# Kernel tuning notes

Measured on AMD Instinct MI355X. Metric: run time of the kernel, lower is better.

Reference implementation:

```python
import jax, jax.numpy as jnp
import numpy as np

N_NODES = 100000
N_EDGES = 640000
H_FEATS = 128


def setup_inputs() -> dict:
    key = jax.random.key(0)
    k_h, k_src, k_dst, k_w1, k_b1, k_w2, k_b2 = jax.random.split(key, 7)
    h = jax.random.normal(k_h, (N_NODES, H_FEATS), dtype=jnp.float32)
    src = jax.random.randint(k_src, (N_EDGES,), 0, N_NODES, dtype=jnp.int64)
    dst = jax.random.randint(k_dst, (N_EDGES,), 0, N_NODES, dtype=jnp.int64)
    # nn.Linear params: W1 (h_feats, 2*h_feats) as (out, in); store transposed for x @ W
    lim1 = 1.0 / np.sqrt(2 * H_FEATS)
    W1 = jax.random.uniform(k_w1, (2 * H_FEATS, H_FEATS), jnp.float32, -lim1, lim1)
    b1 = jax.random.uniform(k_b1, (H_FEATS,), jnp.float32, -lim1, lim1)
    lim2 = 1.0 / np.sqrt(H_FEATS)
    W2 = jax.random.uniform(k_w2, (H_FEATS, 1), jnp.float32, -lim2, lim2)
    b2 = jax.random.uniform(k_b2, (1,), jnp.float32, -lim2, lim2)
    return {"h": h, "src": src, "dst": dst, "W1": W1, "b1": b1, "W2": W2, "b2": b2}


def reference(h, src, dst, W1, b1, W2, b2):
    # gather src/dst node features per edge and concat: [E, 2*h_feats]
    he = jnp.concatenate([h[src], h[dst]], axis=1)
    hidden = jax.nn.relu(he @ W1 + b1)          # [E, h_feats]
    score = (hidden @ W2 + b2)[:, 0]            # [E]
    return score
```

## Files before the change

### kernel.cpp

```cpp
#include <hip/hip_runtime.h>

#define N_NODES 100000
#define N_EDGES 640000
#define F 128
#define NT 6250

typedef __attribute__((ext_vector_type(8))) short short8;
typedef __attribute__((ext_vector_type(4))) float float4v;

static __device__ __forceinline__ unsigned short f2bf(float f) {
    unsigned int u = __float_as_uint(f);
    u += 0x7fffu + ((u >> 16) & 1u);
    return (unsigned short)(u >> 16);
}

__global__ __launch_bounds__(256) void prep_wt(
    const float* __restrict__ W1, unsigned short* __restrict__ Wt)
{
    int id = blockIdx.x * 256 + threadIdx.x;
    int n = id >> 7, k = id & 127;
    float v = W1[((n & 128) + k) * 128 + (n & 127)];
    Wt[id] = f2bf(v);
}

__global__ __launch_bounds__(256, 4) void node_proj(
    const float* __restrict__ h, const unsigned short* __restrict__ Wt,
    const float* __restrict__ b1,
    unsigned short* __restrict__ A, unsigned short* __restrict__ B)
{
    __shared__ unsigned short w_lds[128 * 136];
    __shared__ unsigned short h_lds[4][2][16 * 136];

    const int tid  = threadIdx.x;
    const int lane = tid & 63;
    const int l16  = lane & 15;
    const int quad = lane >> 4;
    const int w    = tid >> 6;
    const int y    = blockIdx.y;

#pragma unroll
    for (int i = 0; i < 8; ++i) {
        int c = i * 256 + tid;
        int r = c >> 4, cc = c & 15;
        uint4 v = *(const uint4*)(Wt + (size_t)(y * 128 + r) * F + cc * 8);
        *(uint4*)&w_lds[r * 136 + cc * 8] = v;
    }
    __syncthreads();

    unsigned short* hb0 = &h_lds[w][0][0];
    unsigned short* hb1 = &h_lds[w][1][0];
    unsigned short* outp = (y == 0) ? A : B;

    int srow[8], sc4[8];
#pragma unroll
    for (int i = 0; i < 8; ++i) { int f = i * 64 + lane; srow[i] = f >> 5; sc4[i] = f & 31; }

#define LOADH(PF, T)                                                           \
    _Pragma("unroll") for (int i = 0; i < 8; ++i)                              \
        PF[i] = *(const float4*)(h + ((size_t)(T) * 16 + srow[i]) * F + sc4[i] * 4);

#define CVTWRITE(PF, DST)                                                      \
    _Pragma("unroll") for (int i = 0; i < 8; ++i) {                            \
        uint2 p;                                                               \
        p.x = (unsigned)f2bf(PF[i].x) | ((unsigned)f2bf(PF[i].y) << 16);       \
        p.y = (unsigned)f2bf(PF[i].z) | ((unsigned)f2bf(PF[i].w) << 16);       \
        *(uint2*)&(DST)[srow[i] * 136 + sc4[i] * 4] = p;                       \
    }

    int t = blockIdx.x * 4 + w;
    bool act = (t < NT);
    float4 pf[8];
    if (act) { LOADH(pf, t); CVTWRITE(pf, hb0); }

    int buf = 0;
    while (act) {
        const int tn = t + 1024;
        const bool actn = (tn < NT);
        if (actn) LOADH(pf, tn);

        unsigned short* hb = buf ? hb1 : hb0;
        float4v acc[8];
#pragma unroll
        for (int mt = 0; mt < 8; ++mt) acc[mt] = (float4v){0.f, 0.f, 0.f, 0.f};
#pragma unroll
        for (int k0 = 0; k0 < 4; ++k0) {
            const int kb = k0 * 32 + quad * 8;
            short8 bf = *(const short8*)&hb[l16 * 136 + kb];
#pragma unroll
            for (int mt = 0; mt < 8; ++mt) {
                short8 af = *(const short8*)&w_lds[(mt * 16 + l16) * 136 + kb];
                acc[mt] = __builtin_amdgcn_mfma_f32_16x16x32_bf16(af, bf, acc[mt], 0, 0, 0);
            }
        }

        if (actn) CVTWRITE(pf, buf ? hb0 : hb1);

        {
            const size_t nodeoff = ((size_t)t * 16 + l16) * F;
#pragma unroll
            for (int mt = 0; mt < 8; ++mt) {
                const int col = mt * 16 + quad * 4;
                float4 bv = make_float4(0.f, 0.f, 0.f, 0.f);
                if (y == 0) bv = *(const float4*)(b1 + col);
                ushort4 sv;
                sv.x = f2bf(acc[mt][0] + bv.x);
                sv.y = f2bf(acc[mt][1] + bv.y);
                sv.z = f2bf(acc[mt][2] + bv.z);
                sv.w = f2bf(acc[mt][3] + bv.w);
                *(ushort4*)(outp + nodeoff + col) = sv;
            }
        }
        buf ^= 1; t = tn; act = actn;
    }
#undef LOADH
#undef CVTWRITE
}

__global__ __launch_bounds__(256) void edge_score(
    const unsigned short* __restrict__ A, const unsigned short* __restrict__ B,
    const int* __restrict__ src, const int* __restrict__ dst,
    const float* __restrict__ W2, const float* __restrict__ b2,
    float* __restrict__ out)
{
    const int tid = threadIdx.x;
    const int sub = tid & 7;
    const int e0  = blockIdx.x * 128 + (tid >> 3) * 4;
    const int j0  = sub * 16;

    const int4 sv = *(const int4*)(src + e0);
    const int4 dv = *(const int4*)(dst + e0);
    const int s[4] = {sv.x, sv.y, sv.z, sv.w};
    const int d[4] = {dv.x, dv.y, dv.z, dv.w};

    uint4 av0[4], av1[4], bv0[4], bv1[4];
#pragma unroll
    for (int i = 0; i < 4; ++i) {
        const uint4* Ap = (const uint4*)(A + (size_t)s[i] * F + j0);
        const uint4* Bp = (const uint4*)(B + (size_t)d[i] * F + j0);
        av0[i] = Ap[0]; av1[i] = Ap[1];
        bv0[i] = Bp[0]; bv1[i] = Bp[1];
    }

    const float4* Wp = (const float4*)(W2 + j0);
    const float4 w0 = Wp[0], w1 = Wp[1], w2 = Wp[2], w3 = Wp[3];
    const float bias = b2[0];

#define TERM(UA, UB, WL, WH)                                                   \
    {                                                                          \
        float fa0 = __uint_as_float((UA) << 16);                               \
        float fa1 = __uint_as_float((UA) & 0xFFFF0000u);                       \
        float fb0 = __uint_as_float((UB) << 16);                               \
        float fb1 = __uint_as_float((UB) & 0xFFFF0000u);                       \
        sacc = fmaf(fmaxf(fa0 + fb0, 0.f), (WL), sacc);                        \
        sacc = fmaf(fmaxf(fa1 + fb1, 0.f), (WH), sacc);                        \
    }
#pragma unroll
    for (int i = 0; i < 4; ++i) {
        float sacc = 0.f;
        TERM(av0[i].x, bv0[i].x, w0.x, w0.y)
        TERM(av0[i].y, bv0[i].y, w0.z, w0.w)
        TERM(av0[i].z, bv0[i].z, w1.x, w1.y)
        TERM(av0[i].w, bv0[i].w, w1.z, w1.w)
        TERM(av1[i].x, bv1[i].x, w2.x, w2.y)
        TERM(av1[i].y, bv1[i].y, w2.z, w2.w)
        TERM(av1[i].z, bv1[i].z, w3.x, w3.y)
        TERM(av1[i].w, bv1[i].w, w3.z, w3.w)
        sacc += __shfl_xor(sacc, 1);
        sacc += __shfl_xor(sacc, 2);
        sacc += __shfl_xor(sacc, 4);
        if (sub == 0) out[e0 + i] = sacc + bias;
    }
#undef TERM
}

extern "C" void kernel_launch(void* const* d_in, const int* in_sizes, int n_in,
                              void* d_out, int out_size, void* d_ws, size_t ws_size,
                              hipStream_t stream) {
    const float* h   = (const float*)d_in[0];
    const int*   src = (const int*)d_in[1];
    const int*   dst = (const int*)d_in[2];
    const float* W1  = (const float*)d_in[3];
    const float* b1  = (const float*)d_in[4];
    const float* W2  = (const float*)d_in[5];
    const float* b2  = (const float*)d_in[6];
    float* out = (float*)d_out;

    unsigned short* Wt = (unsigned short*)d_ws;
    unsigned short* A  = Wt + 256 * 128;
    unsigned short* B  = A + (size_t)N_NODES * F;

    prep_wt<<<128, 256, 0, stream>>>(W1, Wt);
    node_proj<<<dim3(256, 2), 256, 0, stream>>>(h, Wt, b1, A, B);
    edge_score<<<N_EDGES / 128, 256, 0, stream>>>(A, B, src, dst, W2, b2, out);
}
```

Before: 166.1 us.

## Compute both node projections in one block to read h once

node_proj now loads the full 256x128 bf16 weight into LDS and computes both the src-half (A) and dst-half (B) projections for each 16-node tile in a single pass. Previously a second grid dimension computed them separately, so every tile of h was read and converted twice. Blocks grow to 512 threads with one block per CU, and the per-wave h buffer goes from double to single buffering. This trades away some occupancy and double-buffer overlap in exchange for halving the h traffic and conversion work.

```diff
diff --git a/kernel.cpp b/kernel.cpp
--- a/kernel.cpp
+++ b/kernel.cpp
@@ -23,33 +23,35 @@
     Wt[id] = f2bf(v);
 }
 
-__global__ __launch_bounds__(256, 4) void node_proj(
+__global__ __launch_bounds__(512, 1) void node_proj(
     const float* __restrict__ h, const unsigned short* __restrict__ Wt,
     const float* __restrict__ b1,
     unsigned short* __restrict__ A, unsigned short* __restrict__ B)
 {
-    __shared__ unsigned short w_lds[128 * 136];
-    __shared__ unsigned short h_lds[4][2][16 * 136];
+    __shared__ unsigned short w_lds[256 * 136];
+    __shared__ unsigned short h_lds[8][16 * 136 + 8];
 
     const int tid  = threadIdx.x;
     const int lane = tid & 63;
     const int l16  = lane & 15;
     const int quad = lane >> 4;
     const int w    = tid >> 6;
-    const int y    = blockIdx.y;
 
 #pragma unroll
     for (int i = 0; i < 8; ++i) {
-        int c = i * 256 + tid;
+        int c = i * 512 + tid;
         int r = c >> 4, cc = c & 15;
-        uint4 v = *(const uint4*)(Wt + (size_t)(y * 128 + r) * F + cc * 8);
+        uint4 v = *(const uint4*)(Wt + (size_t)r * F + cc * 8);
         *(uint4*)&w_lds[r * 136 + cc * 8] = v;
     }
     __syncthreads();
 
-    unsigned short* hb0 = &h_lds[w][0][0];
-    unsigned short* hb1 = &h_lds[w][1][0];
-    unsigned short* outp = (y == 0) ? A : B;
+    float4 bv[8];
+#pragma unroll
+    for (int mt = 0; mt < 8; ++mt)
+        bv[mt] = *(const float4*)(b1 + mt * 16 + quad * 4);
+
+    unsigned short* hb = &h_lds[w][0];
 
     int srow[8], sc4[8];
 #pragma unroll
@@ -67,50 +69,56 @@
         *(uint2*)&(DST)[srow[i] * 136 + sc4[i] * 4] = p;                       \
     }
 
-    int t = blockIdx.x * 4 + w;
+    int t = blockIdx.x * 8 + w;
     bool act = (t < NT);
     float4 pf[8];
-    if (act) { LOADH(pf, t); CVTWRITE(pf, hb0); }
-
-    int buf = 0;
+    if (act) { LOADH(pf, t); CVTWRITE(pf, hb); }
+
     while (act) {
-        const int tn = t + 1024;
+        const int tn = t + 2048;
         const bool actn = (tn < NT);
         if (actn) LOADH(pf, tn);
 
-        unsigned short* hb = buf ? hb1 : hb0;
-        float4v acc[8];
-#pragma unroll
-        for (int mt = 0; mt < 8; ++mt) acc[mt] = (float4v){0.f, 0.f, 0.f, 0.f};
+        float4v acc[16];
+#pragma unroll
+        for (int mt = 0; mt < 16; ++mt) acc[mt] = (float4v){0.f, 0.f, 0.f, 0.f};
 #pragma unroll
         for (int k0 = 0; k0 < 4; ++k0) {
             const int kb = k0 * 32 + quad * 8;
             short8 bf = *(const short8*)&hb[l16 * 136 + kb];
 #pragma unroll
-            for (int mt = 0; mt < 8; ++mt) {
+            for (int mt = 0; mt < 16; ++mt) {
                 short8 af = *(const short8*)&w_lds[(mt * 16 + l16) * 136 + kb];
                 acc[mt] = __builtin_amdgcn_mfma_f32_16x16x32_bf16(af, bf, acc[mt], 0, 0, 0);
             }
         }
 
-        if (actn) CVTWRITE(pf, buf ? hb0 : hb1);
+        if (actn) CVTWRITE(pf, hb);
 
         {
             const size_t nodeoff = ((size_t)t * 16 + l16) * F;
 #pragma unroll
             for (int mt = 0; mt < 8; ++mt) {
                 const int col = mt * 16 + quad * 4;
-                float4 bv = make_float4(0.f, 0.f, 0.f, 0.f);
-                if (y == 0) bv = *(const float4*)(b1 + col);
                 ushort4 sv;
-                sv.x = f2bf(acc[mt][0] + bv.x);
-                sv.y = f2bf(acc[mt][1] + bv.y);
-                sv.z = f2bf(acc[mt][2] + bv.z);
-                sv.w = f2bf(acc[mt][3] + bv.w);
-                *(ushort4*)(outp + nodeoff + col) = sv;
+                sv.x = f2bf(acc[mt][0] + bv[mt].x);
+                sv.y = f2bf(acc[mt][1] + bv[mt].y);
+                sv.z = f2bf(acc[mt][2] + bv[mt].z);
+                sv.w = f2bf(acc[mt][3] + bv[mt].w);
+                *(ushort4*)(A + nodeoff + col) = sv;
+            }
+#pragma unroll
+            for (int mt = 8; mt < 16; ++mt) {
+                const int col = (mt - 8) * 16 + quad * 4;
+                ushort4 sv;
+                sv.x = f2bf(acc[mt][0]);
+                sv.y = f2bf(acc[mt][1]);
+                sv.z = f2bf(acc[mt][2]);
+                sv.w = f2bf(acc[mt][3]);
+                *(ushort4*)(B + nodeoff + col) = sv;
             }
         }
-        buf ^= 1; t = tn; act = actn;
+        t = tn; act = actn;
     }
 #undef LOADH
 #undef CVTWRITE
@@ -190,6 +198,6 @@
     unsigned short* B  = A + (size_t)N_NODES * F;
 
     prep_wt<<<128, 256, 0, stream>>>(W1, Wt);
-    node_proj<<<dim3(256, 2), 256, 0, stream>>>(h, Wt, b1, A, B);
+    node_proj<<<256, 512, 0, stream>>>(h, Wt, b1, A, B);
     edge_score<<<N_EDGES / 128, 256, 0, stream>>>(A, B, src, dst, W2, b2, out);
 }
```

Measured after the change: 263.1 us. 58.4% more time.

## Share each node tile across A and B projections within one block

Applied to the files above, without the earlier changes.

node_proj now loads the full 256x128 bf16 weight into LDS per block and has all four waves cooperate on one 16-node tile. Two waves produce A columns and two produce B columns, so each h row is read from global memory once instead of twice. The cost is a larger LDS footprint, lower occupancy bounds, and a block-wide barrier every iteration. Bias values are also hoisted out of the loop.

```diff
diff --git a/kernel.cpp b/kernel.cpp
--- a/kernel.cpp
+++ b/kernel.cpp
@@ -4,6 +4,7 @@
 #define N_EDGES 640000
 #define F 128
 #define NT 6250
+#define NBLK 512
 
 typedef __attribute__((ext_vector_type(8))) short short8;
 typedef __attribute__((ext_vector_type(4))) float float4v;
@@ -23,94 +24,96 @@
     Wt[id] = f2bf(v);
 }
 
-__global__ __launch_bounds__(256, 4) void node_proj(
+__global__ __launch_bounds__(256, 2) void node_proj(
     const float* __restrict__ h, const unsigned short* __restrict__ Wt,
     const float* __restrict__ b1,
     unsigned short* __restrict__ A, unsigned short* __restrict__ B)
 {
-    __shared__ unsigned short w_lds[128 * 136];
-    __shared__ unsigned short h_lds[4][2][16 * 136];
+    __shared__ unsigned short w_lds[256 * 136];
+    __shared__ unsigned short h_lds[2][16 * 136];
 
     const int tid  = threadIdx.x;
     const int lane = tid & 63;
     const int l16  = lane & 15;
     const int quad = lane >> 4;
     const int w    = tid >> 6;
-    const int y    = blockIdx.y;
 
 #pragma unroll
-    for (int i = 0; i < 8; ++i) {
+    for (int i = 0; i < 16; ++i) {
         int c = i * 256 + tid;
         int r = c >> 4, cc = c & 15;
-        uint4 v = *(const uint4*)(Wt + (size_t)(y * 128 + r) * F + cc * 8);
+        uint4 v = *(const uint4*)(Wt + (size_t)r * F + cc * 8);
         *(uint4*)&w_lds[r * 136 + cc * 8] = v;
     }
-    __syncthreads();
 
-    unsigned short* hb0 = &h_lds[w][0][0];
-    unsigned short* hb1 = &h_lds[w][1][0];
-    unsigned short* outp = (y == 0) ? A : B;
+    const bool isA = (w < 2);
+    float4 bv[4];
+#pragma unroll
+    for (int p = 0; p < 4; ++p) {
+        int col = (w & 1) * 64 + p * 16 + quad * 4;
+        bv[p] = isA ? *(const float4*)(b1 + col) : make_float4(0.f, 0.f, 0.f, 0.f);
+    }
+    unsigned short* outp = isA ? A : B;
+    const int colb = (w & 1) * 64;
 
-    int srow[8], sc4[8];
+    int srow[2], sc4[2];
 #pragma unroll
-    for (int i = 0; i < 8; ++i) { int f = i * 64 + lane; srow[i] = f >> 5; sc4[i] = f & 31; }
+    for (int i = 0; i < 2; ++i) { int f = i * 256 + tid; srow[i] = f >> 5; sc4[i] = f & 31; }
 
 #define LOADH(PF, T)                                                           \
-    _Pragma("unroll") for (int i = 0; i < 8; ++i)                              \
+    _Pragma("unroll") for (int i = 0; i < 2; ++i)                              \
         PF[i] = *(const float4*)(h + ((size_t)(T) * 16 + srow[i]) * F + sc4[i] * 4);
 
 #define CVTWRITE(PF, DST)                                                      \
-    _Pragma("unroll") for (int i = 0; i < 8; ++i) {                            \
+    _Pragma("unroll") for (int i = 0; i < 2; ++i) {                            \
         uint2 p;                                                               \
         p.x = (unsigned)f2bf(PF[i].x) | ((unsigned)f2bf(PF[i].y) << 16);       \
         p.y = (unsigned)f2bf(PF[i].z) | ((unsigned)f2bf(PF[i].w) << 16);       \
         *(uint2*)&(DST)[srow[i] * 136 + sc4[i] * 4] = p;                       \
     }
 
-    int t = blockIdx.x * 4 + w;
-    bool act = (t < NT);
-    float4 pf[8];
-    if (act) { LOADH(pf, t); CVTWRITE(pf, hb0); }
+    int t = blockIdx.x;
+    float4 pf[2];
+    if (t < NT) { LOADH(pf, t); CVTWRITE(pf, h_lds[0]); }
+    __syncthreads();
 
-    int buf = 0;
-    while (act) {
-        const int tn = t + 1024;
+    int cur = 0;
+    while (t < NT) {
+        const int tn = t + NBLK;
         const bool actn = (tn < NT);
         if (actn) LOADH(pf, tn);
 
-        unsigned short* hb = buf ? hb1 : hb0;
-        float4v acc[8];
+        const unsigned short* hb = h_lds[cur];
+        float4v acc[4];
 #pragma unroll
-        for (int mt = 0; mt < 8; ++mt) acc[mt] = (float4v){0.f, 0.f, 0.f, 0.f};
+        for (int p = 0; p < 4; ++p) acc[p] = (float4v){0.f, 0.f, 0.f, 0.f};
 #pragma unroll
         for (int k0 = 0; k0 < 4; ++k0) {
             const int kb = k0 * 32 + quad * 8;
             short8 bf = *(const short8*)&hb[l16 * 136 + kb];
 #pragma unroll
-            for (int mt = 0; mt < 8; ++mt) {
-                short8 af = *(const short8*)&w_lds[(mt * 16 + l16) * 136 + kb];
-                acc[mt] = __builtin_amdgcn_mfma_f32_16x16x32_bf16(af, bf, acc[mt], 0, 0, 0);
+            for (int p = 0; p < 4; ++p) {
+                short8 af = *(const short8*)&w_lds[(w * 64 + p * 16 + l16) * 136 + kb];
+                acc[p] = __builtin_amdgcn_mfma_f32_16x16x32_bf16(af, bf, acc[p], 0, 0, 0);
             }
         }
 
-        if (actn) CVTWRITE(pf, buf ? hb0 : hb1);
+        if (actn) CVTWRITE(pf, h_lds[cur ^ 1]);
 
         {
             const size_t nodeoff = ((size_t)t * 16 + l16) * F;
 #pragma unroll
-            for (int mt = 0; mt < 8; ++mt) {
-                const int col = mt * 16 + quad * 4;
-                float4 bv = make_float4(0.f, 0.f, 0.f, 0.f);
-                if (y == 0) bv = *(const float4*)(b1 + col);
+            for (int p = 0; p < 4; ++p) {
                 ushort4 sv;
-                sv.x = f2bf(acc[mt][0] + bv.x);
-                sv.y = f2bf(acc[mt][1] + bv.y);
-                sv.z = f2bf(acc[mt][2] + bv.z);
-                sv.w = f2bf(acc[mt][3] + bv.w);
-                *(ushort4*)(outp + nodeoff + col) = sv;
+                sv.x = f2bf(acc[p][0] + bv[p].x);
+                sv.y = f2bf(acc[p][1] + bv[p].y);
+                sv.z = f2bf(acc[p][2] + bv[p].z);
+                sv.w = f2bf(acc[p][3] + bv[p].w);
+                *(ushort4*)(outp + nodeoff + colb + p * 16 + quad * 4) = sv;
             }
         }
-        buf ^= 1; t = tn; act = actn;
+        __syncthreads();
+        cur ^= 1; t = tn;
     }
 #undef LOADH
 #undef CVTWRITE
@@ -190,6 +193,6 @@
     unsigned short* B  = A + (size_t)N_NODES * F;
 
     prep_wt<<<128, 256, 0, stream>>>(W1, Wt);
-    node_proj<<<dim3(256, 2), 256, 0, stream>>>(h, Wt, b1, A, B);
+    node_proj<<<NBLK, 256, 0, stream>>>(h, Wt, b1, A, B);
     edge_score<<<N_EDGES / 128, 256, 0, stream>>>(A, B, src, dst, W2, b2, out);
 }
```

Result: faster. 160.7 us (-3.3%).
